# Optimization experiments

Hardware: AMD Instinct MI355X
Metric: run time of the kernel (lower is better)

Reference implementation:

```python
import jax, jax.numpy as jnp
import numpy as np

N = 640   # nodes
H = 64    # hidden_channels == base feature dim (required by MLP input dims)
DEG = 12  # random directed edges per node before symmetrization


def _mlp(x, Wa, ba, Wb, bb):
    # 2-layer MLP: Linear -> ReLU -> Linear (use_bn=False hardcoded in convs; dropout inactive in eval)
    return jax.nn.relu(x @ Wa + ba) @ Wb + bb


def setup_inputs() -> dict:
    key = jax.random.key(0)
    ks = jax.random.split(key, 8)
    x = jax.random.normal(ks[0], (N, H), dtype=jnp.float32)
    E0 = N * DEG
    src = jax.random.randint(ks[1], (E0,), 0, N)
    dst = jax.random.randint(ks[2], (E0,), 0, N)
    # undirected edge list (both directions), matching PyG k_hop_subgraph semantics on symmetric graphs
    edge_index = jnp.stack([jnp.concatenate([src, dst]), jnp.concatenate([dst, src])])
    batch = jnp.zeros((N,), dtype=jnp.int32)  # unused by the module's forward

    def lin(k, fin, fout):
        kw, kb = jax.random.split(k)
        bound = 1.0 / np.sqrt(fin)
        W = jax.random.uniform(kw, (fin, fout), minval=-bound, maxval=bound, dtype=jnp.float32)
        b = jax.random.uniform(kb, (fout,), minval=-bound, maxval=bound, dtype=jnp.float32)
        return W, b

    W1a, b1a = lin(ks[3], H + 2, H)      # convs[1] mlp: (H+t) -> H
    W1b, b1b = lin(ks[4], H, H + 1)      #               H -> (H+t-1)
    W0a, b0a = lin(ks[5], H + 1, H)      # convs[0] mlp: (H+1) -> H
    W0b, b0b = lin(ks[6], H, H)          #               H -> H
    return dict(x=x, W1a=W1a, b1a=b1a, W1b=W1b, b1b=b1b,
                W0a=W0a, b0a=b0a, W0b=W0b, b0b=b0b,
                edge_index=edge_index, batch=batch)


def reference(x, W1a, b1a, W1b, b1b, W0a, b0a, W0b, b0b, edge_index, batch):
    n = x.shape[0]
    # dense adjacency; self-loops have no effect in the original recursion -> zero diagonal
    A = jnp.zeros((n, n), x.dtype).at[edge_index[0], edge_index[1]].set(1.0)
    A = A * (1.0 - jnp.eye(n, dtype=x.dtype))

    # ---- level 1 (last level, r[1]=1), vectorized over all ego pairs (v, u) ----
    # S2(v,u) = nbrs(u) & S_v (common neighbors of v and u, excluding v, u)
    # sum_{w in S2} x_w  and  |S2|
    Y = A[:, :, None] * x[None, :, :]              # [v, w, d]
    T = jnp.einsum('vwd,uw->vud', Y, A)            # [v, u, d] = sum_w A[v,w] A[u,w] x_w
    cnt = A @ A.T                                  # [v, u] common-neighbor counts
    # hv_u = [x_u, 1, 0]; sum over S2 of [x_w, 1, 1]  ->  GIN input [x_u + T, 1 + cnt, cnt]
    inp1 = jnp.concatenate([x[None, :, :] + T,
                            (1.0 + cnt)[..., None],
                            cnt[..., None]], axis=-1)  # [v, u, H+2]
    out1 = _mlp(inp1, W1a, b1a, W1b, b1b)              # [v, u, H+1]

    # ---- level 0 (r[0]=1): GIN over u in S_v ----
    agg = jnp.einsum('vu,vud->vd', A, out1)            # sum of level-1 embeddings over S_v
    hv = jnp.concatenate([x, jnp.zeros((n, 1), x.dtype)], axis=-1)  # [x_v, 0]
    return _mlp(hv + agg, W0a, b0a, W0b, b0b)          # [N, H]
```

## Files before the change

kernel.cpp:

```cpp
#include <hip/hip_runtime.h>

#define NN   640
#define NW   20
#define NWP  24
#define H    64
#define MAXD 96

__global__ __launch_bounds__(512) void prep(
    const int* __restrict__ ei, int E,
    const float* __restrict__ x,
    const float* __restrict__ W1a, const float* __restrict__ W0a,
    const float* __restrict__ W1b, const float* __restrict__ b1b,
    unsigned* __restrict__ bits, float* __restrict__ xa, float* __restrict__ xc,
    float* __restrict__ Wf, float* __restrict__ bf)
{
    const int t = threadIdx.x, lane = t & 63, wave = t >> 6, bid = blockIdx.x;

    if (bid < 320) {
        __shared__ unsigned sb[2 * NW];
        if (t < 2 * NW) sb[t] = 0u;
        __syncthreads();
        for (int k = t; k < E; k += 512) {
            int a = ei[k];
            if ((a >> 1) == bid) {
                int b = ei[k + E];
                if (b != a) atomicOr(&sb[(a & 1) * NW + (b >> 5)], 1u << (b & 31));
            }
        }
        __syncthreads();
        if (t < 2 * NW) bits[(bid * 2 + t / NW) * NWP + (t % NW)] = sb[t];

        if (wave < 4) {
            const int v = bid * 2 + (wave & 1);
            const float* W = (wave < 2) ? W1a : W0a;
            const float xv = x[v * H + lane];
            float a0 = 0, a1 = 0, a2 = 0, a3 = 0;
            #pragma unroll
            for (int k = 0; k < H; k += 4) {
                a0 += __shfl(xv, k, 64)     * W[k * H + lane];
                a1 += __shfl(xv, k + 1, 64) * W[(k + 1) * H + lane];
                a2 += __shfl(xv, k + 2, 64) * W[(k + 2) * H + lane];
                a3 += __shfl(xv, k + 3, 64) * W[(k + 3) * H + lane];
            }
            float r = (a0 + a1) + (a2 + a3);
            if (wave < 2) xa[v * H + lane] = r; else xc[v * H + lane] = r;
        }
    } else if (bid < 328) {
        const int d = (bid - 320) * 8 + wave;
        const float wv = W1b[d * 65 + lane];
        float a0 = 0, a1 = 0, a2 = 0, a3 = 0;
        #pragma unroll
        for (int e = 0; e < 64; e += 4) {
            a0 += __shfl(wv, e, 64)     * W0a[e * H + lane];
            a1 += __shfl(wv, e + 1, 64) * W0a[(e + 1) * H + lane];
            a2 += __shfl(wv, e + 2, 64) * W0a[(e + 2) * H + lane];
            a3 += __shfl(wv, e + 3, 64) * W0a[(e + 3) * H + lane];
        }
        Wf[d * H + lane] = (a0 + a1) + (a2 + a3) + W1b[d * 65 + 64] * W0a[64 * H + lane];
    } else if (wave == 0) {
        const float bv = b1b[lane];
        float a0 = 0, a1 = 0, a2 = 0, a3 = 0;
        #pragma unroll
        for (int e = 0; e < 64; e += 4) {
            a0 += __shfl(bv, e, 64)     * W0a[e * H + lane];
            a1 += __shfl(bv, e + 1, 64) * W0a[(e + 1) * H + lane];
            a2 += __shfl(bv, e + 2, 64) * W0a[(e + 2) * H + lane];
            a3 += __shfl(bv, e + 3, 64) * W0a[(e + 3) * H + lane];
        }
        bf[lane] = (a0 + a1) + (a2 + a3) + b1b[64] * W0a[64 * H + lane];
    }
}

__global__ __launch_bounds__(512, 6) void fused(
    const float* __restrict__ xa,  const float* __restrict__ xc,
    const float* __restrict__ W1a, const float* __restrict__ b1a,
    const float* __restrict__ Wf,  const float* __restrict__ bf,
    const float* __restrict__ b0a,
    const float* __restrict__ W0b, const float* __restrict__ b0b,
    const unsigned* __restrict__ bits,
    float* __restrict__ out)
{
    __shared__ __align__(16) unsigned rowv[NW];
    __shared__ float xr[MAXD][H];
    __shared__ float p1[8][H];
    __shared__ float p2[8][H];
    __shared__ unsigned short ulist[MAXD];
    __shared__ int pre[NW];
    __shared__ int s_deg;

    const int v = blockIdx.x, t = threadIdx.x;
    const int lane = t & 63, wave = t >> 6;

    if (t < NW) rowv[t] = bits[v * NWP + t];
    __syncthreads();

    if (wave == 0) {
        unsigned word = (lane < NW) ? rowv[lane] : 0u;
        int pc = __popc(word), scan = pc;
        #pragma unroll
        for (int off = 1; off < 32; off <<= 1) {
            int nb = __shfl_up(scan, off, 64);
            if (lane >= off) scan += nb;
        }
        int o = scan - pc;
        if (lane < NW) pre[lane] = o;
        unsigned c = word;
        while (c) {
            int b = __ffs(c) - 1; c &= c - 1;
            if (o < MAXD) ulist[o] = (unsigned short)(lane * 32 + b);
            ++o;
        }
        if (lane == NW - 1) s_deg = (o < MAXD) ? o : MAXD;
    }
    __syncthreads();
    const int deg = s_deg;

    for (int p = wave; p < deg; p += 8)
        xr[p][lane] = xa[ulist[p] * H + lane];

    const float r64 = W1a[64 * H + lane];
    const float k0  = b1a[lane] + r64;
    const float k1  = r64 + W1a[65 * H + lane];

    unsigned rw[NW];
    #pragma unroll
    for (int j = 0; j < NW; ++j) rw[j] = rowv[j];
    __syncthreads();

    float hacc = 0.f;
    for (int p = wave; p < deg; p += 8) {
        const uint4* bu = (const uint4*)(bits + ulist[p] * NWP);
        const uint4 q0 = bu[0], q1 = bu[1], q2 = bu[2], q3 = bu[3], q4 = bu[4];
        unsigned cw[NW] = {
            rw[0]  & q0.x, rw[1]  & q0.y, rw[2]  & q0.z, rw[3]  & q0.w,
            rw[4]  & q1.x, rw[5]  & q1.y, rw[6]  & q1.z, rw[7]  & q1.w,
            rw[8]  & q2.x, rw[9]  & q2.y, rw[10] & q2.z, rw[11] & q2.w,
            rw[12] & q3.x, rw[13] & q3.y, rw[14] & q3.z, rw[15] & q3.w,
            rw[16] & q4.x, rw[17] & q4.y, rw[18] & q4.z, rw[19] & q4.w };
        int cnt = 0;
        #pragma unroll
        for (int j = 0; j < NW; ++j) cnt += __popc(cw[j]);
        float xs = 0.f;
        #pragma unroll
        for (int j = 0; j < NW; ++j) {
            unsigned c = cw[j];
            while (c) {
                int b = __ffs(c) - 1; c &= c - 1;
                int pos = pre[j] + __popc(rw[j] & ((1u << b) - 1));
                xs += xr[pos][lane];
            }
        }
        float h = xr[p][lane] + xs + k0 + (float)cnt * k1;
        hacc += fmaxf(h, 0.f);
    }
    p1[wave][lane] = hacc;
    __syncthreads();

    float hs = 0.f;
    #pragma unroll
    for (int w = 0; w < 8; ++w) hs += p1[w][lane];
    float s = 0.f;
    #pragma unroll
    for (int i = 0; i < 8; ++i) {
        const int d = wave * 8 + i;
        s += __shfl(hs, d, 64) * Wf[d * H + lane];
    }
    p2[wave][lane] = s;
    __syncthreads();

    float s2 = 0.f;
    #pragma unroll
    for (int w = 0; w < 8; ++w) s2 += p2[w][lane];
    const float hh = fmaxf(xc[v * H + lane] + (float)deg * bf[lane]
                           + b0a[lane] + s2, 0.f);
    float o = 0.f;
    #pragma unroll
    for (int i = 0; i < 8; ++i) {
        const int d = wave * 8 + i;
        o += __shfl(hh, d, 64) * W0b[d * H + lane];
    }
    p1[wave][lane] = o;
    __syncthreads();
    if (wave == 0) {
        float oo = b0b[lane];
        #pragma unroll
        for (int w = 0; w < 8; ++w) oo += p1[w][lane];
        out[v * H + lane] = oo;
    }
}

extern "C" void kernel_launch(void* const* d_in, const int* in_sizes, int n_in,
                              void* d_out, int out_size, void* d_ws, size_t ws_size,
                              hipStream_t stream) {
    const float* x   = (const float*)d_in[0];
    const float* W1a = (const float*)d_in[1];
    const float* b1a = (const float*)d_in[2];
    const float* W1b = (const float*)d_in[3];
    const float* b1b = (const float*)d_in[4];
    const float* W0a = (const float*)d_in[5];
    const float* b0a = (const float*)d_in[6];
    const float* W0b = (const float*)d_in[7];
    const float* b0b = (const float*)d_in[8];
    const int*   ei  = (const int*)d_in[9];
    const int    E   = in_sizes[9] / 2;

    char* ws = (char*)d_ws;
    unsigned* bits = (unsigned*)(ws);
    float*    xa   = (float*)(ws + 61440);
    float*    xc   = (float*)(ws + 61440 + 163840);
    float*    Wf   = (float*)(ws + 61440 + 2 * 163840);
    float*    bf   = (float*)(ws + 61440 + 2 * 163840 + 16384);

    prep<<<329, 512, 0, stream>>>(ei, E, x, W1a, W0a, W1b, b1b, bits, xa, xc, Wf, bf);
    fused<<<NN, 512, 0, stream>>>(xa, xc, W1a, b1a, Wf, bf, b0a, W0b, b0b,
                                  bits, (float*)d_out);
}
```

Measured before the change: 24.54 us.

## Build adjacency bitsets with 4 nodes per block and stage neighbor rows in LDS

The prep kernel now has each block own 4 nodes instead of 2 and scans the edge list with int4 vector loads. This halves the number of blocks that each re-read the whole edge list and overlaps the x@W projections with the scan. In the fused kernel, the neighbor bitset rows are copied cooperatively into shared memory before the intersection loop, replacing per-wave uint4 global loads with LDS reads. The cost is extra LDS usage (about 7.5KB), which may lower occupancy, and an added staging pass.

```diff
diff --git a/kernel.cpp b/kernel.cpp
--- a/kernel.cpp
+++ b/kernel.cpp
@@ -16,37 +16,51 @@
 {
     const int t = threadIdx.x, lane = t & 63, wave = t >> 6, bid = blockIdx.x;
 
-    if (bid < 320) {
-        __shared__ unsigned sb[2 * NW];
-        if (t < 2 * NW) sb[t] = 0u;
+    if (bid < 160) {
+        __shared__ unsigned sb[4 * NW];
+        if (t < 4 * NW) sb[t] = 0u;
         __syncthreads();
-        for (int k = t; k < E; k += 512) {
-            int a = ei[k];
-            if ((a >> 1) == bid) {
-                int b = ei[k + E];
-                if (b != a) atomicOr(&sb[(a & 1) * NW + (b >> 5)], 1u << (b & 31));
+
+        const int quads = E >> 2;
+        for (int k = t; k < quads; k += 512) {
+            const int4 a4 = ((const int4*)ei)[k];
+            if ((a4.x >> 2) == bid || (a4.y >> 2) == bid ||
+                (a4.z >> 2) == bid || (a4.w >> 2) == bid) {
+                const int4 b4 = ((const int4*)(ei + E))[k];
+                if ((a4.x >> 2) == bid && a4.x != b4.x)
+                    atomicOr(&sb[(a4.x & 3) * NW + (b4.x >> 5)], 1u << (b4.x & 31));
+                if ((a4.y >> 2) == bid && a4.y != b4.y)
+                    atomicOr(&sb[(a4.y & 3) * NW + (b4.y >> 5)], 1u << (b4.y & 31));
+                if ((a4.z >> 2) == bid && a4.z != b4.z)
+                    atomicOr(&sb[(a4.z & 3) * NW + (b4.z >> 5)], 1u << (b4.z & 31));
+                if ((a4.w >> 2) == bid && a4.w != b4.w)
+                    atomicOr(&sb[(a4.w & 3) * NW + (b4.w >> 5)], 1u << (b4.w & 31));
             }
         }
+        for (int k = (quads << 2) + t; k < E; k += 512) {
+            const int a = ei[k], b = ei[k + E];
+            if ((a >> 2) == bid && a != b)
+                atomicOr(&sb[(a & 3) * NW + (b >> 5)], 1u << (b & 31));
+        }
+
+        const int v = bid * 4 + (wave >> 1);
+        const float* W = (wave & 1) ? W0a : W1a;
+        const float xv = x[v * H + lane];
+        float a0 = 0, a1 = 0, a2 = 0, a3 = 0;
+        #pragma unroll
+        for (int k = 0; k < H; k += 4) {
+            a0 += __shfl(xv, k, 64)     * W[k * H + lane];
+            a1 += __shfl(xv, k + 1, 64) * W[(k + 1) * H + lane];
+            a2 += __shfl(xv, k + 2, 64) * W[(k + 2) * H + lane];
+            a3 += __shfl(xv, k + 3, 64) * W[(k + 3) * H + lane];
+        }
+        float r = (a0 + a1) + (a2 + a3);
+        if (wave & 1) xc[v * H + lane] = r; else xa[v * H + lane] = r;
+
         __syncthreads();
-        if (t < 2 * NW) bits[(bid * 2 + t / NW) * NWP + (t % NW)] = sb[t];
-
-        if (wave < 4) {
-            const int v = bid * 2 + (wave & 1);
-            const float* W = (wave < 2) ? W1a : W0a;
-            const float xv = x[v * H + lane];
-            float a0 = 0, a1 = 0, a2 = 0, a3 = 0;
-            #pragma unroll
-            for (int k = 0; k < H; k += 4) {
-                a0 += __shfl(xv, k, 64)     * W[k * H + lane];
-                a1 += __shfl(xv, k + 1, 64) * W[(k + 1) * H + lane];
-                a2 += __shfl(xv, k + 2, 64) * W[(k + 2) * H + lane];
-                a3 += __shfl(xv, k + 3, 64) * W[(k + 3) * H + lane];
-            }
-            float r = (a0 + a1) + (a2 + a3);
-            if (wave < 2) xa[v * H + lane] = r; else xc[v * H + lane] = r;
-        }
-    } else if (bid < 328) {
-        const int d = (bid - 320) * 8 + wave;
+        if (t < 4 * NW) bits[(bid * 4 + t / NW) * NWP + (t % NW)] = sb[t];
+    } else if (bid < 168) {
+        const int d = (bid - 160) * 8 + wave;
         const float wv = W1b[d * 65 + lane];
         float a0 = 0, a1 = 0, a2 = 0, a3 = 0;
         #pragma unroll
@@ -81,6 +95,7 @@
     float* __restrict__ out)
 {
     __shared__ __align__(16) unsigned rowv[NW];
+    __shared__ __align__(16) unsigned nbs[MAXD * NW];
     __shared__ float xr[MAXD][H];
     __shared__ float p1[8][H];
     __shared__ float p2[8][H];
@@ -117,6 +132,10 @@
 
     for (int p = wave; p < deg; p += 8)
         xr[p][lane] = xa[ulist[p] * H + lane];
+    for (int idx = t; idx < deg * NW; idx += 512) {
+        const int p = idx / NW, w = idx - p * NW;
+        nbs[p * NW + w] = bits[ulist[p] * NWP + w];
+    }
 
     const float r64 = W1a[64 * H + lane];
     const float k0  = b1a[lane] + r64;
@@ -129,7 +148,7 @@
 
     float hacc = 0.f;
     for (int p = wave; p < deg; p += 8) {
-        const uint4* bu = (const uint4*)(bits + ulist[p] * NWP);
+        const uint4* bu = (const uint4*)(nbs + p * NW);
         const uint4 q0 = bu[0], q1 = bu[1], q2 = bu[2], q3 = bu[3], q4 = bu[4];
         unsigned cw[NW] = {
             rw[0]  & q0.x, rw[1]  & q0.y, rw[2]  & q0.z, rw[3]  & q0.w,
@@ -211,7 +230,7 @@
     float*    Wf   = (float*)(ws + 61440 + 2 * 163840);
     float*    bf   = (float*)(ws + 61440 + 2 * 163840 + 16384);
 
-    prep<<<329, 512, 0, stream>>>(ei, E, x, W1a, W0a, W1b, b1b, bits, xa, xc, Wf, bf);
+    prep<<<169, 512, 0, stream>>>(ei, E, x, W1a, W0a, W1b, b1b, bits, xa, xc, Wf, bf);
     fused<<<NN, 512, 0, stream>>>(xa, xc, W1a, b1a, Wf, bf, b0a, W0b, b0b,
                                   bits, (float*)d_out);
 }
```

Measured after the change: 20.77 us. 1.18x faster.
